# Performance work log

Measured on AMD Instinct MI355X. Metric: run time of the kernel, lower is better.

Reference implementation:

```python
import jax, jax.numpy as jnp
import numpy as np

COMMITMENT_COST = 0.25


def l2norm(x, eps=1e-12):
    # F.normalize along last dim
    n = jnp.linalg.norm(x, axis=-1, keepdims=True)
    return x / jnp.maximum(n, eps)


def vector_quantize(x, codebook, commitment_cost):
    """Euclidean VQ: cdist + argmin, straight-through, VQ loss + perplexity.
    x: (B, N, D), codebook: (K, D)."""
    B, N, D = x.shape
    K = codebook.shape[0]
    flat = x.reshape(-1, D)  # (BN, D)
    # squared euclidean distances via expansion (no (BN,K,D) intermediate)
    d = (jnp.sum(flat * flat, axis=-1, keepdims=True)
         - 2.0 * flat @ codebook.T
         + jnp.sum(codebook * codebook, axis=-1))  # (BN, K)
    idx = jnp.argmin(d, axis=-1)  # (BN,)
    q = codebook[idx]  # (BN, D)
    # VQ losses
    e_latent = jnp.mean((jax.lax.stop_gradient(q) - flat) ** 2)
    q_latent = jnp.mean((q - jax.lax.stop_gradient(flat)) ** 2)
    loss = q_latent + commitment_cost * e_latent
    # perplexity over codebook usage (bincount, not dense one-hot)
    counts = jnp.zeros((K,), flat.dtype).at[idx].add(1.0)
    probs = counts / idx.shape[0]
    perplexity = jnp.exp(-jnp.sum(probs * jnp.log(probs + 1e-10)))
    return idx.reshape(B, N), perplexity, loss


def transform_mfcc(X):
    # wave_embedding.transform_freq: normalize frames, then rfft -> real -> bins 2:40
    Xn = l2norm(X)
    spec = jnp.fft.rfft(Xn, axis=-1).real[..., 2:40]  # (B, N, 38)
    return l2norm(spec)  # mfcc_embedding.norm_fn


def setup_inputs() -> dict:
    key = jax.random.key(0)
    k1, k2, k3 = jax.random.split(key, 3)
    X = jax.random.normal(k1, (16, 4096, 80), dtype=jnp.float32)
    wave_codebook = jax.random.normal(k2, (1024, 80), dtype=jnp.float32)
    mfcc_codebook = jax.random.normal(k3, (256, 38), dtype=jnp.float32)
    return {"X": X, "wave_codebook": wave_codebook, "mfcc_codebook": mfcc_codebook}


def reference(X, wave_codebook, mfcc_codebook):
    K_wave = wave_codebook.shape[0]
    wave_idx, wave_ppl, wave_loss = vector_quantize(X, wave_codebook, COMMITMENT_COST)
    X_mfcc = transform_mfcc(X)
    mfcc_idx, mfcc_ppl, mfcc_loss = vector_quantize(X_mfcc, mfcc_codebook, COMMITMENT_COST)
    mfcc_idx = mfcc_idx + K_wave
    # rearrange stack([wave, mfcc], dim=1): 'b c n -> b (n c)' -> interleave per frame
    B, N = wave_idx.shape
    encodings = jnp.stack([wave_idx, mfcc_idx], axis=-1).reshape(B, 2 * N)
    return encodings, wave_ppl, wave_loss, mfcc_ppl, mfcc_loss
```

## Files before the change

kernel.cpp:

```cpp
#include <hip/hip_runtime.h>
#include <hip/hip_bf16.h>
#include <math.h>


#define NROWS 65536
#define DW    80
#define KW    1024
#define DM    38
#define KM    256

typedef __attribute__((ext_vector_type(8))) short bf16x8;
typedef __attribute__((ext_vector_type(4))) float f32x4;

__device__ __forceinline__ void bf16split(float v, short& h, short& l) {
    __hip_bfloat16 hb = __float2bfloat16(v);
    float hf = __bfloat162float(hb);
    __hip_bfloat16 lb = __float2bfloat16(v - hf);
    h = *(short*)&hb;
    l = *(short*)&lb;
}

__device__ __forceinline__ void bf16split3(float v, short& a, short& b, short& c) {
    __hip_bfloat16 h = __float2bfloat16(v);
    float hf = __bfloat162float(h);
    float r = v - hf;
    __hip_bfloat16 m = __float2bfloat16(r);
    float mf = __bfloat162float(m);
    __hip_bfloat16 lo = __float2bfloat16(r - mf);
    a = *(short*)&h; b = *(short*)&m; c = *(short*)&lo;
}

__device__ __forceinline__ bf16x8 bf8zero() {
    bf16x8 z;
    #pragma unroll
    for (int j = 0; j < 8; ++j) z[j] = 0;
    return z;
}

#define WS_SUMS   0
#define WS_HIST   256
#define WS_CNW    5376
#define WS_CNM    9472
#define WS_CTF    10496
#define WS_CBF    33536
#define WS_CWH    107264
#define WS_CWL    303872

__global__ __launch_bounds__(256) void prep_kernel(
    const float* __restrict__ cbw, const float* __restrict__ cbm,
    float* __restrict__ sums, int* __restrict__ hist,
    float* __restrict__ cn_w, float* __restrict__ cn_m,
    short* __restrict__ ctf, short* __restrict__ cbf,
    short* __restrict__ cwh, short* __restrict__ cwl)
{
    int idx = blockIdx.x * 256 + threadIdx.x;
    if (idx < 12288) {
        const int f = idx;
        const int ct = f / 192, rem = f % 192, s = rem >> 6, l = rem & 63;
        const int code = ct * 16 + (l & 15);
        const int k0 = 32 * s + 8 * (l >> 4);
        bf16x8 h, lo;
        if (k0 < DW) {
            const float4* p = (const float4*)(cbw + (size_t)code * DW + k0);
            float4 u = p[0], v = p[1];
            float fv[8] = {u.x, u.y, u.z, u.w, v.x, v.y, v.z, v.w};
            #pragma unroll
            for (int j = 0; j < 8; ++j) {
                short hh, ll;
                bf16split(fv[j], hh, ll);
                h[j] = hh; lo[j] = ll;
            }
        } else { h = bf8zero(); lo = bf8zero(); }
        *(bf16x8*)&cwh[(size_t)f * 8] = h;
        *(bf16x8*)&cwl[(size_t)f * 8] = lo;
    } else if (idx < 16128) {
        int t = idx - 12288;
        int col, k;
        if (t < 3072) {
            int j = t & 7, l = (t >> 3) & 63, tt = t >> 9;
            col = (tt >> 1) * 16 + (l & 15);
            k = 32 * (tt & 1) + 8 * (l >> 4) + j;
        } else {
            int i2 = t - 3072;
            int j = i2 & 7, l = (i2 >> 3) & 31, ct = i2 >> 8;
            col = ct * 16 + (l & 15);
            k = 64 + 8 * (l >> 4) + j;
        }
        float v = (col < DM)
            ? (float)cos(2.0 * 3.14159265358979323846 * (double)((col + 2) * k) / 80.0)
            : 0.f;
        short a, b, c; bf16split3(v, a, b, c);
        ctf[t] = a; ctf[3840 + t] = b; ctf[7680 + t] = c;
    } else if (idx < 28416) {
        int i3 = idx - 16128;
        int code, k;
        if (i3 < 8192) {
            int j = i3 & 7, l = (i3 >> 3) & 63, ct = i3 >> 9;
            code = ct * 16 + (l & 15);
            k = 8 * (l >> 4) + j;
        } else {
            int i4 = i3 - 8192;
            int j = i4 & 7, l = (i4 >> 3) & 31, ct = i4 >> 8;
            code = ct * 16 + (l & 15);
            k = 32 + 8 * (l >> 4) + j;
        }
        float v = (k < DM) ? cbm[(size_t)code * DM + k] : 0.f;
        short a, b, c; bf16split3(v, a, b, c);
        cbf[i3] = a; cbf[12288 + i3] = b; cbf[24576 + i3] = c;
    } else if (idx < 29440) {
        int i = idx - 28416;
        const float* p = cbw + (size_t)i * DW;
        float s = 0.f;
        for (int k = 0; k < DW; ++k) s = fmaf(p[k], p[k], s);
        cn_w[i] = s;
    } else if (idx < 29696) {
        int i = idx - 29440;
        const float* p = cbm + (size_t)i * DM;
        float s = 0.f;
        for (int j = 0; j < DM; ++j) s = fmaf(p[j], p[j], s);
        cn_m[i] = s;
    } else if (idx < 30976) {
        hist[idx - 29696] = 0;
    } else if (idx == 30976) sums[0] = 0.f;
    else if (idx == 30977)   sums[1] = 0.f;
}

__global__ __launch_bounds__(256, 2) void wave_vq_mfma(
    const float* __restrict__ X, const short* __restrict__ cwh,
    const short* __restrict__ cwl, const float* __restrict__ cn,
    float* __restrict__ out, float* __restrict__ sums)
{
    __shared__ float redw[4];

    const int tid = threadIdx.x;
    const int l   = tid & 63;
    const int qu  = tid >> 6;
    const int c16 = l & 15;
    const int g   = l >> 4;
    const size_t rowbase = (size_t)blockIdx.x * 256 + (size_t)qu * 64;

    bf16x8 Ah[4][3], Al[4][3];
    float xs2[4] = {0.f, 0.f, 0.f, 0.f};
    #pragma unroll
    for (int rt = 0; rt < 4; ++rt) {
        #pragma unroll
        for (int s = 0; s < 3; ++s) {
            const int k0 = 32 * s + 8 * g;
            bf16x8 ah, al;
            if (k0 < DW) {
                const float4* ap =
                    (const float4*)(X + (rowbase + rt * 16 + c16) * DW + k0);
                float4 u = ap[0], w = ap[1];
                float f[8] = {u.x, u.y, u.z, u.w, w.x, w.y, w.z, w.w};
                #pragma unroll
                for (int j = 0; j < 8; ++j) {
                    short hh, ll;
                    bf16split(f[j], hh, ll);
                    ah[j] = hh; al[j] = ll;
                    xs2[rt] = fmaf(f[j], f[j], xs2[rt]);
                }
            } else {
                ah = bf8zero(); al = bf8zero();
            }
            Ah[rt][s] = ah; Al[rt][s] = al;
        }
    }
    #pragma unroll
    for (int rt = 0; rt < 4; ++rt) {
        xs2[rt] += __shfl_xor(xs2[rt], 16, 64);
        xs2[rt] += __shfl_xor(xs2[rt], 32, 64);
    }

    float bd[4][4];
    int   bi[4][4];
    #pragma unroll
    for (int rt = 0; rt < 4; ++rt)
        #pragma unroll
        for (int i = 0; i < 4; ++i) { bd[rt][i] = 3.4e38f; bi[rt][i] = 0; }

    const bf16x8* Hsrc = (const bf16x8*)cwh;
    const bf16x8* Lsrc = (const bf16x8*)cwl;

    bf16x8 pbh[3], pbl[3];
    #pragma unroll
    for (int s = 0; s < 3; ++s) {
        pbh[s] = Hsrc[s * 64 + l];
        pbl[s] = Lsrc[s * 64 + l];
    }
    float pcn = cn[c16];

    #pragma unroll 1
    for (int ct = 0; ct < 64; ++ct) {
        bf16x8 bh[3], bl[3];
        #pragma unroll
        for (int s = 0; s < 3; ++s) { bh[s] = pbh[s]; bl[s] = pbl[s]; }
        const float cnv = pcn;
        if (ct < 63) {
            #pragma unroll
            for (int s = 0; s < 3; ++s) {
                pbh[s] = Hsrc[((ct + 1) * 3 + s) * 64 + l];
                pbl[s] = Lsrc[((ct + 1) * 3 + s) * 64 + l];
            }
            pcn = cn[(ct + 1) * 16 + c16];
        }

        f32x4 acc[4];
        #pragma unroll
        for (int rt = 0; rt < 4; ++rt) acc[rt] = (f32x4){0.f, 0.f, 0.f, 0.f};
        #pragma unroll
        for (int s = 0; s < 3; ++s) {
            #pragma unroll
            for (int rt = 0; rt < 4; ++rt)
                acc[rt] = __builtin_amdgcn_mfma_f32_16x16x32_bf16(Al[rt][s], bl[s], acc[rt], 0, 0, 0);
            #pragma unroll
            for (int rt = 0; rt < 4; ++rt)
                acc[rt] = __builtin_amdgcn_mfma_f32_16x16x32_bf16(Ah[rt][s], bl[s], acc[rt], 0, 0, 0);
            #pragma unroll
            for (int rt = 0; rt < 4; ++rt)
                acc[rt] = __builtin_amdgcn_mfma_f32_16x16x32_bf16(Al[rt][s], bh[s], acc[rt], 0, 0, 0);
            #pragma unroll
            for (int rt = 0; rt < 4; ++rt)
                acc[rt] = __builtin_amdgcn_mfma_f32_16x16x32_bf16(Ah[rt][s], bh[s], acc[rt], 0, 0, 0);
        }
        const int idxbase = ct * 16 + c16;
        #pragma unroll
        for (int rt = 0; rt < 4; ++rt) {
            #pragma unroll
            for (int i = 0; i < 4; ++i) {
                float d = fmaf(-2.f, acc[rt][i], cnv);
                if (d < bd[rt][i]) { bd[rt][i] = d; bi[rt][i] = idxbase; }
            }
        }
    }

    float lw = 0.f;
    #pragma unroll
    for (int rt = 0; rt < 4; ++rt) {
        #pragma unroll
        for (int i = 0; i < 4; ++i) {
            float d = bd[rt][i]; int ix = bi[rt][i];
            #pragma unroll
            for (int m = 1; m < 16; m <<= 1) {
                float d2 = __shfl_xor(d, m, 64);
                int   i2 = __shfl_xor(ix, m, 64);
                if (d2 < d || (d2 == d && i2 < ix)) { d = d2; ix = i2; }
            }
            float xn = __shfl(xs2[rt], (l & 48) + 4 * (l >> 4) + i, 64);
            if (c16 == 0) {
                size_t row = rowbase + rt * 16 + 4 * g + i;
                out[2 * row] = (float)ix;
                lw += d + xn;
            }
        }
    }
    #pragma unroll
    for (int m = 1; m < 64; m <<= 1) lw += __shfl_xor(lw, m, 64);
    if (l == 0) redw[qu] = lw;
    __syncthreads();
    if (tid == 0) atomicAdd(&sums[0], redw[0] + redw[1] + redw[2] + redw[3]);
}

__global__ __launch_bounds__(256, 2) void mfcc_mfma(
    const float* __restrict__ X, const float* __restrict__ cn_m,
    const short* __restrict__ ctf, const short* __restrict__ cbf,
    float* __restrict__ out, float* __restrict__ sums)
{
    __shared__ float XF[4][64 * 49];
    __shared__ float CN[KM];
    __shared__ float red4[4];

    const int tid = threadIdx.x;
    const int l   = tid & 63;
    const int w   = tid >> 6;
    const int c16 = l & 15;
    const int g   = l >> 4;
    const size_t rowbase = (size_t)blockIdx.x * 256 + (size_t)w * 64;

    if (tid < KM) CN[tid] = cn_m[tid];
    __syncthreads();

    float* xfl = &XF[w][0];

    #pragma unroll 1
    for (int rt = 0; rt < 4; ++rt) {
        bf16x8 A0[3], A1[3], A2[3];
        #pragma unroll
        for (int s = 0; s < 3; ++s) {
            const int k0 = 32 * s + 8 * g;
            if (k0 < DW) {
                const float4* ap =
                    (const float4*)(X + (rowbase + rt * 16 + c16) * DW + k0);
                float4 u = ap[0], v = ap[1];
                float f[8] = {u.x, u.y, u.z, u.w, v.x, v.y, v.z, v.w};
                bf16x8 a0, a1, a2;
                #pragma unroll
                for (int j = 0; j < 8; ++j) {
                    short aa, bb, cc;
                    bf16split3(f[j], aa, bb, cc);
                    a0[j] = aa; a1[j] = bb; a2[j] = cc;
                }
                A0[s] = a0; A1[s] = a1; A2[s] = a2;
            } else {
                A0[s] = bf8zero(); A1[s] = bf8zero(); A2[s] = bf8zero();
            }
        }

        f32x4 acc[3];
        #pragma unroll
        for (int ct = 0; ct < 3; ++ct) acc[ct] = (f32x4){0.f, 0.f, 0.f, 0.f};

        #pragma unroll
        for (int s = 0; s < 3; ++s) {
            #pragma unroll
            for (int ct = 0; ct < 3; ++ct) {
                bf16x8 b0, b1, b2;
                if (s < 2) {
                    const int off = ((ct * 2 + s) * 64 + l) * 8;
                    b0 = *(const bf16x8*)&ctf[off];
                    b1 = *(const bf16x8*)&ctf[3840 + off];
                    b2 = *(const bf16x8*)&ctf[7680 + off];
                } else if (l < 32) {
                    const int off = 3072 + (ct * 32 + l) * 8;
                    b0 = *(const bf16x8*)&ctf[off];
                    b1 = *(const bf16x8*)&ctf[3840 + off];
                    b2 = *(const bf16x8*)&ctf[7680 + off];
                } else {
                    b0 = bf8zero(); b1 = bf8zero(); b2 = bf8zero();
                }
                acc[ct] = __builtin_amdgcn_mfma_f32_16x16x32_bf16(A2[s], b0, acc[ct], 0, 0, 0);
                acc[ct] = __builtin_amdgcn_mfma_f32_16x16x32_bf16(A1[s], b1, acc[ct], 0, 0, 0);
                acc[ct] = __builtin_amdgcn_mfma_f32_16x16x32_bf16(A0[s], b2, acc[ct], 0, 0, 0);
                acc[ct] = __builtin_amdgcn_mfma_f32_16x16x32_bf16(A1[s], b0, acc[ct], 0, 0, 0);
                acc[ct] = __builtin_amdgcn_mfma_f32_16x16x32_bf16(A0[s], b1, acc[ct], 0, 0, 0);
                acc[ct] = __builtin_amdgcn_mfma_f32_16x16x32_bf16(A0[s], b0, acc[ct], 0, 0, 0);
            }
        }

        #pragma unroll
        for (int i = 0; i < 4; ++i) {
            float n2 = acc[0][i] * acc[0][i];
            n2 = fmaf(acc[1][i], acc[1][i], n2);
            n2 = fmaf(acc[2][i], acc[2][i], n2);
            #pragma unroll
            for (int m = 1; m < 16; m <<= 1) n2 += __shfl_xor(n2, m, 64);
            float inv = 1.0f / fmaxf(sqrtf(n2), 1e-12f);
            const int row_l = rt * 16 + 4 * g + i;
            #pragma unroll
            for (int ct = 0; ct < 3; ++ct)
                xfl[row_l * 49 + ct * 16 + c16] = acc[ct][i] * inv;
        }
    }
    __syncthreads();

    bf16x8 X0[4][3], X1[4][3];
    #pragma unroll
    for (int rt = 0; rt < 4; ++rt) {
        const int r0 = rt * 16 + c16;
        {
            const float* p = &xfl[r0 * 49 + 8 * g];
            bf16x8 q0, q1, q2;
            #pragma unroll
            for (int j = 0; j < 8; ++j) {
                short aa, bb, cc;
                bf16split3(p[j], aa, bb, cc);
                q0[j] = aa; q1[j] = bb; q2[j] = cc;
            }
            X0[rt][0] = q0; X0[rt][1] = q1; X0[rt][2] = q2;
        }
        if (g < 2) {
            const float* p = &xfl[r0 * 49 + 32 + 8 * g];
            bf16x8 q0, q1, q2;
            #pragma unroll
            for (int j = 0; j < 8; ++j) {
                short aa, bb, cc;
                bf16split3(p[j], aa, bb, cc);
                q0[j] = aa; q1[j] = bb; q2[j] = cc;
            }
            X1[rt][0] = q0; X1[rt][1] = q1; X1[rt][2] = q2;
        } else {
            X1[rt][0] = bf8zero(); X1[rt][1] = bf8zero(); X1[rt][2] = bf8zero();
        }
    }

    float bd[4][4];
    int   bi[4][4];
    #pragma unroll
    for (int rt = 0; rt < 4; ++rt)
        #pragma unroll
        for (int i = 0; i < 4; ++i) { bd[rt][i] = 3.4e38f; bi[rt][i] = 0; }

    #pragma unroll 1
    for (int ct = 0; ct < 16; ++ct) {
        bf16x8 B0[3], B1[3];
        const int off0 = (ct * 64 + l) * 8;
        B0[0] = *(const bf16x8*)&cbf[off0];
        B0[1] = *(const bf16x8*)&cbf[12288 + off0];
        B0[2] = *(const bf16x8*)&cbf[24576 + off0];
        if (l < 32) {
            const int off1 = 8192 + (ct * 32 + l) * 8;
            B1[0] = *(const bf16x8*)&cbf[off1];
            B1[1] = *(const bf16x8*)&cbf[12288 + off1];
            B1[2] = *(const bf16x8*)&cbf[24576 + off1];
        } else {
            B1[0] = bf8zero(); B1[1] = bf8zero(); B1[2] = bf8zero();
        }
        const float cnv = CN[ct * 16 + c16];
        const int idxbase = ct * 16 + c16;
        #pragma unroll
        for (int rt = 0; rt < 4; ++rt) {
            f32x4 a = (f32x4){0.f, 0.f, 0.f, 0.f};
            a = __builtin_amdgcn_mfma_f32_16x16x32_bf16(X0[rt][2], B0[0], a, 0, 0, 0);
            a = __builtin_amdgcn_mfma_f32_16x16x32_bf16(X0[rt][1], B0[1], a, 0, 0, 0);
            a = __builtin_amdgcn_mfma_f32_16x16x32_bf16(X0[rt][0], B0[2], a, 0, 0, 0);
            a = __builtin_amdgcn_mfma_f32_16x16x32_bf16(X1[rt][2], B1[0], a, 0, 0, 0);
            a = __builtin_amdgcn_mfma_f32_16x16x32_bf16(X1[rt][1], B1[1], a, 0, 0, 0);
            a = __builtin_amdgcn_mfma_f32_16x16x32_bf16(X1[rt][0], B1[2], a, 0, 0, 0);
            a = __builtin_amdgcn_mfma_f32_16x16x32_bf16(X0[rt][1], B0[0], a, 0, 0, 0);
            a = __builtin_amdgcn_mfma_f32_16x16x32_bf16(X0[rt][0], B0[1], a, 0, 0, 0);
            a = __builtin_amdgcn_mfma_f32_16x16x32_bf16(X1[rt][1], B1[0], a, 0, 0, 0);
            a = __builtin_amdgcn_mfma_f32_16x16x32_bf16(X1[rt][0], B1[1], a, 0, 0, 0);
            a = __builtin_amdgcn_mfma_f32_16x16x32_bf16(X0[rt][0], B0[0], a, 0, 0, 0);
            a = __builtin_amdgcn_mfma_f32_16x16x32_bf16(X1[rt][0], B1[0], a, 0, 0, 0);
            #pragma unroll
            for (int i = 0; i < 4; ++i) {
                float d = fmaf(-2.f, a[i], cnv);
                if (d < bd[rt][i]) { bd[rt][i] = d; bi[rt][i] = idxbase; }
            }
        }
    }

    float lm = 0.f;
    #pragma unroll
    for (int rt = 0; rt < 4; ++rt) {
        #pragma unroll
        for (int i = 0; i < 4; ++i) {
            float d = bd[rt][i]; int ix = bi[rt][i];
            #pragma unroll
            for (int m = 1; m < 16; m <<= 1) {
                float d2 = __shfl_xor(d, m, 64);
                int   i2 = __shfl_xor(ix, m, 64);
                if (d2 < d || (d2 == d && i2 < ix)) { d = d2; ix = i2; }
            }
            if (c16 == 0) {
                size_t row = rowbase + rt * 16 + 4 * g + i;
                out[2 * row + 1] = (float)(ix + KW);
                lm += d + 1.0f;
            }
        }
    }
    #pragma unroll
    for (int m = 1; m < 64; m <<= 1) lm += __shfl_xor(lm, m, 64);
    if (l == 0) red4[w] = lm;
    __syncthreads();
    if (tid == 0) atomicAdd(&sums[1], red4[0] + red4[1] + red4[2] + red4[3]);
}

__global__ __launch_bounds__(256) void hist_kernel(
    const float* __restrict__ out, int* __restrict__ hist)
{
    __shared__ int h[1280];
    const int tid = threadIdx.x;
    for (int i = tid; i < 1280; i += 256) h[i] = 0;
    __syncthreads();
    const int base = blockIdx.x * 1024;
    for (int rr = tid; rr < 1024; rr += 256) {
        const int r = base + rr;
        atomicAdd(&h[(int)out[2 * r]], 1);
        atomicAdd(&h[1024 + ((int)out[2 * r + 1] - KW)], 1);
    }
    __syncthreads();
    for (int i = tid; i < 1280; i += 256)
        if (h[i]) atomicAdd(&hist[i], h[i]);
}

__global__ __launch_bounds__(256) void finalize_kernel(
    const int* __restrict__ hist, const float* __restrict__ sums,
    float* __restrict__ out)
{
    __shared__ float red[4];
    const int tid = threadIdx.x;
    const bool wv = (blockIdx.x == 0);
    const int K = wv ? KW : KM;
    const int base = wv ? 0 : 1024;
    float s = 0.f;
    for (int i = tid; i < K; i += 256) {
        float p = (float)hist[base + i] * (1.0f / 65536.0f);
        s += p * logf(p + 1e-10f);
    }
    #pragma unroll
    for (int off = 32; off >= 1; off >>= 1) s += __shfl_xor(s, off, 64);
    if ((tid & 63) == 0) red[tid >> 6] = s;
    __syncthreads();
    if (tid == 0) {
        float t = red[0] + red[1] + red[2] + red[3];
        float ppl = expf(-t);
        float denom = wv ? (float)(NROWS * DW) : (float)(NROWS * DM);
        int obase = 2 * NROWS + (wv ? 0 : 2);
        out[obase]     = ppl;
        out[obase + 1] = 1.25f * sums[wv ? 0 : 1] / denom;
    }
}

extern "C" void kernel_launch(void* const* d_in, const int* in_sizes, int n_in,
                              void* d_out, int out_size, void* d_ws, size_t ws_size,
                              hipStream_t stream) {
    const float* X   = (const float*)d_in[0];
    const float* cbw = (const float*)d_in[1];
    const float* cbm = (const float*)d_in[2];
    float* out = (float*)d_out;

    char* ws = (char*)d_ws;
    float* sums = (float*)(ws + WS_SUMS);
    int*   hist = (int*)(ws + WS_HIST);
    float* cn_w = (float*)(ws + WS_CNW);
    float* cn_m = (float*)(ws + WS_CNM);
    short* ctf  = (short*)(ws + WS_CTF);
    short* cbf  = (short*)(ws + WS_CBF);
    short* cwh  = (short*)(ws + WS_CWH);
    short* cwl  = (short*)(ws + WS_CWL);

    prep_kernel<<<122, 256, 0, stream>>>(cbw, cbm, sums, hist, cn_w, cn_m,
                                         ctf, cbf, cwh, cwl);
    wave_vq_mfma<<<NROWS / 256, 256, 0, stream>>>(X, cwh, cwl, cn_w, out, sums);
    mfcc_mfma<<<NROWS / 256, 256, 0, stream>>>(X, cn_m, ctf, cbf, out, sums);
    hist_kernel<<<64, 256, 0, stream>>>(out, hist);
    finalize_kernel<<<2, 256, 0, stream>>>(hist, sums, out);
}
```

Measured before the change: 94.13 us.

## Split codebook search across wave pairs and double the grid size

Both VQ kernels now have two waves share each 64-row group. Each wave scans half of the codebook tiles, and the partial argmins are merged through shared memory before the index write and the loss reduction. Blocks now cover 128 rows instead of 256, so twice as many blocks are launched. The intent is to fill the GPU's compute units with more resident waves. The costs are duplicated X loads and bf16 splitting across the pair, an extra LDS exchange, and a block barrier. In the mfcc kernel the explicit barrier after the CN load was removed, so correctness depends on a later barrier before CN is read.

```diff
diff --git a/kernel.cpp b/kernel.cpp
--- a/kernel.cpp
+++ b/kernel.cpp
@@ -130,14 +130,18 @@
     const short* __restrict__ cwl, const float* __restrict__ cn,
     float* __restrict__ out, float* __restrict__ sums)
 {
-    __shared__ float redw[4];
-
-    const int tid = threadIdx.x;
-    const int l   = tid & 63;
-    const int qu  = tid >> 6;
-    const int c16 = l & 15;
-    const int g   = l >> 4;
-    const size_t rowbase = (size_t)blockIdx.x * 256 + (size_t)qu * 64;
+    __shared__ float sd[2][64][16];
+    __shared__ int   si[2][64][16];
+    __shared__ float redw[2];
+
+    const int tid  = threadIdx.x;
+    const int l    = tid & 63;
+    const int qu   = tid >> 6;
+    const int grp  = qu >> 1;
+    const int half = qu & 1;
+    const int c16  = l & 15;
+    const int g    = l >> 4;
+    const size_t rowbase = (size_t)blockIdx.x * 128 + (size_t)grp * 64;
 
     bf16x8 Ah[4][3], Al[4][3];
     float xs2[4] = {0.f, 0.f, 0.f, 0.f};
@@ -180,22 +184,24 @@
 
     const bf16x8* Hsrc = (const bf16x8*)cwh;
     const bf16x8* Lsrc = (const bf16x8*)cwl;
+    const int ct0 = half * 32;
 
     bf16x8 pbh[3], pbl[3];
     #pragma unroll
     for (int s = 0; s < 3; ++s) {
-        pbh[s] = Hsrc[s * 64 + l];
-        pbl[s] = Lsrc[s * 64 + l];
-    }
-    float pcn = cn[c16];
+        pbh[s] = Hsrc[(ct0 * 3 + s) * 64 + l];
+        pbl[s] = Lsrc[(ct0 * 3 + s) * 64 + l];
+    }
+    float pcn = cn[ct0 * 16 + c16];
 
     #pragma unroll 1
-    for (int ct = 0; ct < 64; ++ct) {
+    for (int ctl = 0; ctl < 32; ++ctl) {
+        const int ct = ct0 + ctl;
         bf16x8 bh[3], bl[3];
         #pragma unroll
         for (int s = 0; s < 3; ++s) { bh[s] = pbh[s]; bl[s] = pbl[s]; }
         const float cnv = pcn;
-        if (ct < 63) {
+        if (ctl < 31) {
             #pragma unroll
             for (int s = 0; s < 3; ++s) {
                 pbh[s] = Hsrc[((ct + 1) * 3 + s) * 64 + l];
@@ -233,31 +239,46 @@
         }
     }
 
-    float lw = 0.f;
-    #pragma unroll
-    for (int rt = 0; rt < 4; ++rt) {
-        #pragma unroll
-        for (int i = 0; i < 4; ++i) {
-            float d = bd[rt][i]; int ix = bi[rt][i];
-            #pragma unroll
-            for (int m = 1; m < 16; m <<= 1) {
-                float d2 = __shfl_xor(d, m, 64);
-                int   i2 = __shfl_xor(ix, m, 64);
-                if (d2 < d || (d2 == d && i2 < ix)) { d = d2; ix = i2; }
-            }
-            float xn = __shfl(xs2[rt], (l & 48) + 4 * (l >> 4) + i, 64);
-            if (c16 == 0) {
-                size_t row = rowbase + rt * 16 + 4 * g + i;
-                out[2 * row] = (float)ix;
-                lw += d + xn;
-            }
-        }
-    }
-    #pragma unroll
-    for (int m = 1; m < 64; m <<= 1) lw += __shfl_xor(lw, m, 64);
-    if (l == 0) redw[qu] = lw;
-    __syncthreads();
-    if (tid == 0) atomicAdd(&sums[0], redw[0] + redw[1] + redw[2] + redw[3]);
+    if (half == 1) {
+        #pragma unroll
+        for (int rt = 0; rt < 4; ++rt)
+            #pragma unroll
+            for (int i = 0; i < 4; ++i) {
+                sd[grp][l][rt * 4 + i] = bd[rt][i];
+                si[grp][l][rt * 4 + i] = bi[rt][i];
+            }
+    }
+    __syncthreads();
+    if (half == 0) {
+        float lw = 0.f;
+        #pragma unroll
+        for (int rt = 0; rt < 4; ++rt) {
+            #pragma unroll
+            for (int i = 0; i < 4; ++i) {
+                float d = bd[rt][i]; int ix = bi[rt][i];
+                float dp = sd[grp][l][rt * 4 + i];
+                int   ip = si[grp][l][rt * 4 + i];
+                if (dp < d || (dp == d && ip < ix)) { d = dp; ix = ip; }
+                #pragma unroll
+                for (int m = 1; m < 16; m <<= 1) {
+                    float d2 = __shfl_xor(d, m, 64);
+                    int   i2 = __shfl_xor(ix, m, 64);
+                    if (d2 < d || (d2 == d && i2 < ix)) { d = d2; ix = i2; }
+                }
+                float xn = __shfl(xs2[rt], (l & 48) + 4 * (l >> 4) + i, 64);
+                if (c16 == 0) {
+                    size_t row = rowbase + rt * 16 + 4 * g + i;
+                    out[2 * row] = (float)ix;
+                    lw += d + xn;
+                }
+            }
+        }
+        #pragma unroll
+        for (int m = 1; m < 64; m <<= 1) lw += __shfl_xor(lw, m, 64);
+        if (l == 0) redw[grp] = lw;
+    }
+    __syncthreads();
+    if (tid == 0) atomicAdd(&sums[0], redw[0] + redw[1]);
 }
 
 __global__ __launch_bounds__(256, 2) void mfcc_mfma(
@@ -265,24 +286,28 @@
     const short* __restrict__ ctf, const short* __restrict__ cbf,
     float* __restrict__ out, float* __restrict__ sums)
 {
-    __shared__ float XF[4][64 * 49];
+    __shared__ float XF[2][64 * 49];
+    __shared__ float sd[2][64][16];
+    __shared__ int   si[2][64][16];
     __shared__ float CN[KM];
-    __shared__ float red4[4];
-
-    const int tid = threadIdx.x;
-    const int l   = tid & 63;
-    const int w   = tid >> 6;
-    const int c16 = l & 15;
-    const int g   = l >> 4;
-    const size_t rowbase = (size_t)blockIdx.x * 256 + (size_t)w * 64;
+    __shared__ float red2[2];
+
+    const int tid  = threadIdx.x;
+    const int l    = tid & 63;
+    const int qu   = tid >> 6;
+    const int grp  = qu >> 1;
+    const int half = qu & 1;
+    const int c16  = l & 15;
+    const int g    = l >> 4;
+    const size_t rowbase = (size_t)blockIdx.x * 128 + (size_t)grp * 64;
 
     if (tid < KM) CN[tid] = cn_m[tid];
-    __syncthreads();
-
-    float* xfl = &XF[w][0];
+
+    float* xfl = &XF[grp][0];
 
     #pragma unroll 1
-    for (int rt = 0; rt < 4; ++rt) {
+    for (int rt2 = 0; rt2 < 2; ++rt2) {
+        const int rt = half * 2 + rt2;
         bf16x8 A0[3], A1[3], A2[3];
         #pragma unroll
         for (int s = 0; s < 3; ++s) {
@@ -390,7 +415,8 @@
         for (int i = 0; i < 4; ++i) { bd[rt][i] = 3.4e38f; bi[rt][i] = 0; }
 
     #pragma unroll 1
-    for (int ct = 0; ct < 16; ++ct) {
+    for (int ctl = 0; ctl < 8; ++ctl) {
+        const int ct = half * 8 + ctl;
         bf16x8 B0[3], B1[3];
         const int off0 = (ct * 64 + l) * 8;
         B0[0] = *(const bf16x8*)&cbf[off0];
@@ -429,30 +455,45 @@
         }
     }
 
-    float lm = 0.f;
-    #pragma unroll
-    for (int rt = 0; rt < 4; ++rt) {
-        #pragma unroll
-        for (int i = 0; i < 4; ++i) {
-            float d = bd[rt][i]; int ix = bi[rt][i];
-            #pragma unroll
-            for (int m = 1; m < 16; m <<= 1) {
-                float d2 = __shfl_xor(d, m, 64);
-                int   i2 = __shfl_xor(ix, m, 64);
-                if (d2 < d || (d2 == d && i2 < ix)) { d = d2; ix = i2; }
-            }
-            if (c16 == 0) {
-                size_t row = rowbase + rt * 16 + 4 * g + i;
-                out[2 * row + 1] = (float)(ix + KW);
-                lm += d + 1.0f;
-            }
-        }
-    }
-    #pragma unroll
-    for (int m = 1; m < 64; m <<= 1) lm += __shfl_xor(lm, m, 64);
-    if (l == 0) red4[w] = lm;
-    __syncthreads();
-    if (tid == 0) atomicAdd(&sums[1], red4[0] + red4[1] + red4[2] + red4[3]);
+    if (half == 1) {
+        #pragma unroll
+        for (int rt = 0; rt < 4; ++rt)
+            #pragma unroll
+            for (int i = 0; i < 4; ++i) {
+                sd[grp][l][rt * 4 + i] = bd[rt][i];
+                si[grp][l][rt * 4 + i] = bi[rt][i];
+            }
+    }
+    __syncthreads();
+    if (half == 0) {
+        float lm = 0.f;
+        #pragma unroll
+        for (int rt = 0; rt < 4; ++rt) {
+            #pragma unroll
+            for (int i = 0; i < 4; ++i) {
+                float d = bd[rt][i]; int ix = bi[rt][i];
+                float dp = sd[grp][l][rt * 4 + i];
+                int   ip = si[grp][l][rt * 4 + i];
+                if (dp < d || (dp == d && ip < ix)) { d = dp; ix = ip; }
+                #pragma unroll
+                for (int m = 1; m < 16; m <<= 1) {
+                    float d2 = __shfl_xor(d, m, 64);
+                    int   i2 = __shfl_xor(ix, m, 64);
+                    if (d2 < d || (d2 == d && i2 < ix)) { d = d2; ix = i2; }
+                }
+                if (c16 == 0) {
+                    size_t row = rowbase + rt * 16 + 4 * g + i;
+                    out[2 * row + 1] = (float)(ix + KW);
+                    lm += d + 1.0f;
+                }
+            }
+        }
+        #pragma unroll
+        for (int m = 1; m < 64; m <<= 1) lm += __shfl_xor(lm, m, 64);
+        if (l == 0) red2[grp] = lm;
+    }
+    __syncthreads();
+    if (tid == 0) atomicAdd(&sums[1], red2[0] + red2[1]);
 }
 
 __global__ __launch_bounds__(256) void hist_kernel(
@@ -521,8 +562,8 @@
 
     prep_kernel<<<122, 256, 0, stream>>>(cbw, cbm, sums, hist, cn_w, cn_m,
                                          ctf, cbf, cwh, cwl);
-    wave_vq_mfma<<<NROWS / 256, 256, 0, stream>>>(X, cwh, cwl, cn_w, out, sums);
-    mfcc_mfma<<<NROWS / 256, 256, 0, stream>>>(X, cn_m, ctf, cbf, out, sums);
+    wave_vq_mfma<<<NROWS / 128, 256, 0, stream>>>(X, cwh, cwl, cn_w, out, sums);
+    mfcc_mfma<<<NROWS / 128, 256, 0, stream>>>(X, cn_m, ctf, cbf, out, sums);
     hist_kernel<<<64, 256, 0, stream>>>(out, hist);
     finalize_kernel<<<2, 256, 0, stream>>>(hist, sums, out);
 }
```

New measurement: 89.73 us. -4.7%, faster.

## Shrink per-wave row tiles to one 16-row tile and raise occupancy

Applied to the files above, without the earlier changes.

Each wave in the wave and mfcc VQ kernels now handles a single 16-row tile instead of four. The grids grow to match (512-thread wave blocks with periodic barriers, smaller mfcc blocks with reduced shared memory), and the histogram kernel gets one row per thread. The aim is to cut register and LDS pressure so more waves fit per CU and more blocks spread across the many CUs. The cost is less reuse of each codebook fragment load across rows, so codebook traffic per row rises about fourfold.

```diff
diff --git a/kernel.cpp b/kernel.cpp
--- a/kernel.cpp
+++ b/kernel.cpp
@@ -35,6 +35,51 @@
     #pragma unroll
     for (int j = 0; j < 8; ++j) z[j] = 0;
     return z;
+}
+
+__device__ __forceinline__ void wvq_tile(
+    const bf16x8 (&Ah)[3], const bf16x8 (&Al)[3],
+    const bf16x8 (&bh)[3], const bf16x8 (&bl)[3],
+    float cnv, int idx0, float (&bd)[4], int (&bi)[4])
+{
+    f32x4 acc = (f32x4){0.f, 0.f, 0.f, 0.f};
+    #pragma unroll
+    for (int s = 0; s < 3; ++s) {
+        acc = __builtin_amdgcn_mfma_f32_16x16x32_bf16(Al[s], bl[s], acc, 0, 0, 0);
+        acc = __builtin_amdgcn_mfma_f32_16x16x32_bf16(Ah[s], bl[s], acc, 0, 0, 0);
+        acc = __builtin_amdgcn_mfma_f32_16x16x32_bf16(Al[s], bh[s], acc, 0, 0, 0);
+        acc = __builtin_amdgcn_mfma_f32_16x16x32_bf16(Ah[s], bh[s], acc, 0, 0, 0);
+    }
+    #pragma unroll
+    for (int i = 0; i < 4; ++i) {
+        float d = fmaf(-2.f, acc[i], cnv);
+        if (d < bd[i]) { bd[i] = d; bi[i] = idx0; }
+    }
+}
+
+__device__ __forceinline__ void mvq_tile(
+    const bf16x8 (&X0)[3], const bf16x8 (&X1)[3],
+    const bf16x8 (&B0)[3], const bf16x8 (&B1)[3],
+    float cnv, int idx0, float (&bd)[4], int (&bi)[4])
+{
+    f32x4 a = (f32x4){0.f, 0.f, 0.f, 0.f};
+    a = __builtin_amdgcn_mfma_f32_16x16x32_bf16(X0[2], B0[0], a, 0, 0, 0);
+    a = __builtin_amdgcn_mfma_f32_16x16x32_bf16(X0[1], B0[1], a, 0, 0, 0);
+    a = __builtin_amdgcn_mfma_f32_16x16x32_bf16(X0[0], B0[2], a, 0, 0, 0);
+    a = __builtin_amdgcn_mfma_f32_16x16x32_bf16(X1[2], B1[0], a, 0, 0, 0);
+    a = __builtin_amdgcn_mfma_f32_16x16x32_bf16(X1[1], B1[1], a, 0, 0, 0);
+    a = __builtin_amdgcn_mfma_f32_16x16x32_bf16(X1[0], B1[2], a, 0, 0, 0);
+    a = __builtin_amdgcn_mfma_f32_16x16x32_bf16(X0[1], B0[0], a, 0, 0, 0);
+    a = __builtin_amdgcn_mfma_f32_16x16x32_bf16(X0[0], B0[1], a, 0, 0, 0);
+    a = __builtin_amdgcn_mfma_f32_16x16x32_bf16(X1[1], B1[0], a, 0, 0, 0);
+    a = __builtin_amdgcn_mfma_f32_16x16x32_bf16(X1[0], B1[1], a, 0, 0, 0);
+    a = __builtin_amdgcn_mfma_f32_16x16x32_bf16(X0[0], B0[0], a, 0, 0, 0);
+    a = __builtin_amdgcn_mfma_f32_16x16x32_bf16(X1[0], B1[0], a, 0, 0, 0);
+    #pragma unroll
+    for (int i = 0; i < 4; ++i) {
+        float d = fmaf(-2.f, a[i], cnv);
+        if (d < bd[i]) { bd[i] = d; bi[i] = idx0; }
+    }
 }
 
 #define WS_SUMS   0
@@ -125,269 +170,217 @@
     else if (idx == 30977)   sums[1] = 0.f;
 }
 
-__global__ __launch_bounds__(256, 2) void wave_vq_mfma(
+__global__ __launch_bounds__(512, 4) void wave_vq_mfma(
     const float* __restrict__ X, const short* __restrict__ cwh,
     const short* __restrict__ cwl, const float* __restrict__ cn,
     float* __restrict__ out, float* __restrict__ sums)
 {
-    __shared__ float redw[4];
+    __shared__ float redw[8];
 
     const int tid = threadIdx.x;
     const int l   = tid & 63;
     const int qu  = tid >> 6;
     const int c16 = l & 15;
     const int g   = l >> 4;
-    const size_t rowbase = (size_t)blockIdx.x * 256 + (size_t)qu * 64;
-
-    bf16x8 Ah[4][3], Al[4][3];
-    float xs2[4] = {0.f, 0.f, 0.f, 0.f};
-    #pragma unroll
-    for (int rt = 0; rt < 4; ++rt) {
+    const size_t rowbase = (size_t)blockIdx.x * 128 + (size_t)qu * 16;
+
+    bf16x8 Ah[3], Al[3];
+    float xs2 = 0.f;
+    #pragma unroll
+    for (int s = 0; s < 3; ++s) {
+        const int k0 = 32 * s + 8 * g;
+        bf16x8 ah, al;
+        if (k0 < DW) {
+            const float4* ap = (const float4*)(X + (rowbase + c16) * DW + k0);
+            float4 u = ap[0], w = ap[1];
+            float f[8] = {u.x, u.y, u.z, u.w, w.x, w.y, w.z, w.w};
+            #pragma unroll
+            for (int j = 0; j < 8; ++j) {
+                short hh, ll;
+                bf16split(f[j], hh, ll);
+                ah[j] = hh; al[j] = ll;
+                xs2 = fmaf(f[j], f[j], xs2);
+            }
+        } else { ah = bf8zero(); al = bf8zero(); }
+        Ah[s] = ah; Al[s] = al;
+    }
+    xs2 += __shfl_xor(xs2, 16, 64);
+    xs2 += __shfl_xor(xs2, 32, 64);
+
+    float bd[4]; int bi[4];
+    #pragma unroll
+    for (int i = 0; i < 4; ++i) { bd[i] = 3.4e38f; bi[i] = 0; }
+
+    const bf16x8* Hp = (const bf16x8*)cwh + l;
+    const bf16x8* Lp = (const bf16x8*)cwl + l;
+
+    bf16x8 b0h[3], b0l[3], b1h[3], b1l[3];
+    float cn0, cn1;
+    #pragma unroll
+    for (int s = 0; s < 3; ++s) { b0h[s] = Hp[s * 64]; b0l[s] = Lp[s * 64]; }
+    cn0 = cn[c16];
+
+    #pragma unroll 1
+    for (int ct = 0; ct < 64; ct += 2) {
+        if ((ct & 15) == 0) __syncthreads();
         #pragma unroll
         for (int s = 0; s < 3; ++s) {
-            const int k0 = 32 * s + 8 * g;
-            bf16x8 ah, al;
-            if (k0 < DW) {
-                const float4* ap =
-                    (const float4*)(X + (rowbase + rt * 16 + c16) * DW + k0);
-                float4 u = ap[0], w = ap[1];
-                float f[8] = {u.x, u.y, u.z, u.w, w.x, w.y, w.z, w.w};
-                #pragma unroll
-                for (int j = 0; j < 8; ++j) {
-                    short hh, ll;
-                    bf16split(f[j], hh, ll);
-                    ah[j] = hh; al[j] = ll;
-                    xs2[rt] = fmaf(f[j], f[j], xs2[rt]);
-                }
-            } else {
-                ah = bf8zero(); al = bf8zero();
-            }
-            Ah[rt][s] = ah; Al[rt][s] = al;
-        }
-    }
-    #pragma unroll
-    for (int rt = 0; rt < 4; ++rt) {
-        xs2[rt] += __shfl_xor(xs2[rt], 16, 64);
-        xs2[rt] += __shfl_xor(xs2[rt], 32, 64);
-    }
-
-    float bd[4][4];
-    int   bi[4][4];
-    #pragma unroll
-    for (int rt = 0; rt < 4; ++rt)
-        #pragma unroll
-        for (int i = 0; i < 4; ++i) { bd[rt][i] = 3.4e38f; bi[rt][i] = 0; }
-
-    const bf16x8* Hsrc = (const bf16x8*)cwh;
-    const bf16x8* Lsrc = (const bf16x8*)cwl;
-
-    bf16x8 pbh[3], pbl[3];
-    #pragma unroll
-    for (int s = 0; s < 3; ++s) {
-        pbh[s] = Hsrc[s * 64 + l];
-        pbl[s] = Lsrc[s * 64 + l];
-    }
-    float pcn = cn[c16];
-
-    #pragma unroll 1
-    for (int ct = 0; ct < 64; ++ct) {
-        bf16x8 bh[3], bl[3];
-        #pragma unroll
-        for (int s = 0; s < 3; ++s) { bh[s] = pbh[s]; bl[s] = pbl[s]; }
-        const float cnv = pcn;
-        if (ct < 63) {
+            b1h[s] = Hp[((ct + 1) * 3 + s) * 64];
+            b1l[s] = Lp[((ct + 1) * 3 + s) * 64];
+        }
+        cn1 = cn[(ct + 1) * 16 + c16];
+        wvq_tile(Ah, Al, b0h, b0l, cn0, ct * 16 + c16, bd, bi);
+        if (ct + 2 < 64) {
             #pragma unroll
             for (int s = 0; s < 3; ++s) {
-                pbh[s] = Hsrc[((ct + 1) * 3 + s) * 64 + l];
-                pbl[s] = Lsrc[((ct + 1) * 3 + s) * 64 + l];
+                b0h[s] = Hp[((ct + 2) * 3 + s) * 64];
+                b0l[s] = Lp[((ct + 2) * 3 + s) * 64];
             }
-            pcn = cn[(ct + 1) * 16 + c16];
-        }
-
-        f32x4 acc[4];
-        #pragma unroll
-        for (int rt = 0; rt < 4; ++rt) acc[rt] = (f32x4){0.f, 0.f, 0.f, 0.f};
-        #pragma unroll
-        for (int s = 0; s < 3; ++s) {
-            #pragma unroll
-            for (int rt = 0; rt < 4; ++rt)
-                acc[rt] = __builtin_amdgcn_mfma_f32_16x16x32_bf16(Al[rt][s], bl[s], acc[rt], 0, 0, 0);
-            #pragma unroll
-            for (int rt = 0; rt < 4; ++rt)
-                acc[rt] = __builtin_amdgcn_mfma_f32_16x16x32_bf16(Ah[rt][s], bl[s], acc[rt], 0, 0, 0);
-            #pragma unroll
-            for (int rt = 0; rt < 4; ++rt)
-                acc[rt] = __builtin_amdgcn_mfma_f32_16x16x32_bf16(Al[rt][s], bh[s], acc[rt], 0, 0, 0);
-            #pragma unroll
-            for (int rt = 0; rt < 4; ++rt)
-                acc[rt] = __builtin_amdgcn_mfma_f32_16x16x32_bf16(Ah[rt][s], bh[s], acc[rt], 0, 0, 0);
-        }
-        const int idxbase = ct * 16 + c16;
-        #pragma unroll
-        for (int rt = 0; rt < 4; ++rt) {
-            #pragma unroll
-            for (int i = 0; i < 4; ++i) {
-                float d = fmaf(-2.f, acc[rt][i], cnv);
-                if (d < bd[rt][i]) { bd[rt][i] = d; bi[rt][i] = idxbase; }
-            }
-        }
+            cn0 = cn[(ct + 2) * 16 + c16];
+        }
+        wvq_tile(Ah, Al, b1h, b1l, cn1, (ct + 1) * 16 + c16, bd, bi);
     }
 
     float lw = 0.f;
     #pragma unroll
-    for (int rt = 0; rt < 4; ++rt) {
-        #pragma unroll
-        for (int i = 0; i < 4; ++i) {
-            float d = bd[rt][i]; int ix = bi[rt][i];
-            #pragma unroll
-            for (int m = 1; m < 16; m <<= 1) {
-                float d2 = __shfl_xor(d, m, 64);
-                int   i2 = __shfl_xor(ix, m, 64);
-                if (d2 < d || (d2 == d && i2 < ix)) { d = d2; ix = i2; }
-            }
-            float xn = __shfl(xs2[rt], (l & 48) + 4 * (l >> 4) + i, 64);
-            if (c16 == 0) {
-                size_t row = rowbase + rt * 16 + 4 * g + i;
-                out[2 * row] = (float)ix;
-                lw += d + xn;
-            }
+    for (int i = 0; i < 4; ++i) {
+        float d = bd[i]; int ix = bi[i];
+        #pragma unroll
+        for (int m = 1; m < 16; m <<= 1) {
+            float d2 = __shfl_xor(d, m, 64);
+            int   i2 = __shfl_xor(ix, m, 64);
+            if (d2 < d || (d2 == d && i2 < ix)) { d = d2; ix = i2; }
+        }
+        float xn = __shfl(xs2, (l & 48) + 4 * g + i, 64);
+        if (c16 == 0) {
+            size_t row = rowbase + 4 * g + i;
+            out[2 * row] = (float)ix;
+            lw += d + xn;
         }
     }
     #pragma unroll
     for (int m = 1; m < 64; m <<= 1) lw += __shfl_xor(lw, m, 64);
     if (l == 0) redw[qu] = lw;
     __syncthreads();
-    if (tid == 0) atomicAdd(&sums[0], redw[0] + redw[1] + redw[2] + redw[3]);
-}
-
-__global__ __launch_bounds__(256, 2) void mfcc_mfma(
+    if (tid == 0) {
+        float t = 0.f;
+        #pragma unroll
+        for (int q = 0; q < 8; ++q) t += redw[q];
+        atomicAdd(&sums[0], t);
+    }
+}
+
+__global__ __launch_bounds__(256, 4) void mfcc_mfma(
     const float* __restrict__ X, const float* __restrict__ cn_m,
     const short* __restrict__ ctf, const short* __restrict__ cbf,
     float* __restrict__ out, float* __restrict__ sums)
 {
-    __shared__ float XF[4][64 * 49];
+    __shared__ float XF[4][16 * 52];
     __shared__ float CN[KM];
     __shared__ float red4[4];
 
     const int tid = threadIdx.x;
     const int l   = tid & 63;
-    const int w   = tid >> 6;
+    const int qu  = tid >> 6;
     const int c16 = l & 15;
     const int g   = l >> 4;
-    const size_t rowbase = (size_t)blockIdx.x * 256 + (size_t)w * 64;
-
-    if (tid < KM) CN[tid] = cn_m[tid];
-    __syncthreads();
-
-    float* xfl = &XF[w][0];
-
-    #pragma unroll 1
-    for (int rt = 0; rt < 4; ++rt) {
-        bf16x8 A0[3], A1[3], A2[3];
-        #pragma unroll
-        for (int s = 0; s < 3; ++s) {
-            const int k0 = 32 * s + 8 * g;
-            if (k0 < DW) {
-                const float4* ap =
-                    (const float4*)(X + (rowbase + rt * 16 + c16) * DW + k0);
-                float4 u = ap[0], v = ap[1];
-                float f[8] = {u.x, u.y, u.z, u.w, v.x, v.y, v.z, v.w};
-                bf16x8 a0, a1, a2;
-                #pragma unroll
-                for (int j = 0; j < 8; ++j) {
-                    short aa, bb, cc;
-                    bf16split3(f[j], aa, bb, cc);
-                    a0[j] = aa; a1[j] = bb; a2[j] = cc;
-                }
-                A0[s] = a0; A1[s] = a1; A2[s] = a2;
-            } else {
-                A0[s] = bf8zero(); A1[s] = bf8zero(); A2[s] = bf8zero();
-            }
-        }
-
-        f32x4 acc[3];
-        #pragma unroll
-        for (int ct = 0; ct < 3; ++ct) acc[ct] = (f32x4){0.f, 0.f, 0.f, 0.f};
-
-        #pragma unroll
-        for (int s = 0; s < 3; ++s) {
-            #pragma unroll
-            for (int ct = 0; ct < 3; ++ct) {
-                bf16x8 b0, b1, b2;
-                if (s < 2) {
-                    const int off = ((ct * 2 + s) * 64 + l) * 8;
-                    b0 = *(const bf16x8*)&ctf[off];
-                    b1 = *(const bf16x8*)&ctf[3840 + off];
-                    b2 = *(const bf16x8*)&ctf[7680 + off];
-                } else if (l < 32) {
-                    const int off = 3072 + (ct * 32 + l) * 8;
-                    b0 = *(const bf16x8*)&ctf[off];
-                    b1 = *(const bf16x8*)&ctf[3840 + off];
-                    b2 = *(const bf16x8*)&ctf[7680 + off];
-                } else {
-                    b0 = bf8zero(); b1 = bf8zero(); b2 = bf8zero();
-                }
-                acc[ct] = __builtin_amdgcn_mfma_f32_16x16x32_bf16(A2[s], b0, acc[ct], 0, 0, 0);
-                acc[ct] = __builtin_amdgcn_mfma_f32_16x16x32_bf16(A1[s], b1, acc[ct], 0, 0, 0);
-                acc[ct] = __builtin_amdgcn_mfma_f32_16x16x32_bf16(A0[s], b2, acc[ct], 0, 0, 0);
-                acc[ct] = __builtin_amdgcn_mfma_f32_16x16x32_bf16(A1[s], b0, acc[ct], 0, 0, 0);
-                acc[ct] = __builtin_amdgcn_mfma_f32_16x16x32_bf16(A0[s], b1, acc[ct], 0, 0, 0);
-                acc[ct] = __builtin_amdgcn_mfma_f32_16x16x32_bf16(A0[s], b0, acc[ct], 0, 0, 0);
-            }
-        }
-
-        #pragma unroll
-        for (int i = 0; i < 4; ++i) {
-            float n2 = acc[0][i] * acc[0][i];
-            n2 = fmaf(acc[1][i], acc[1][i], n2);
-            n2 = fmaf(acc[2][i], acc[2][i], n2);
-            #pragma unroll
-            for (int m = 1; m < 16; m <<= 1) n2 += __shfl_xor(n2, m, 64);
-            float inv = 1.0f / fmaxf(sqrtf(n2), 1e-12f);
-            const int row_l = rt * 16 + 4 * g + i;
-            #pragma unroll
-            for (int ct = 0; ct < 3; ++ct)
-                xfl[row_l * 49 + ct * 16 + c16] = acc[ct][i] * inv;
-        }
-    }
-    __syncthreads();
-
-    bf16x8 X0[4][3], X1[4][3];
-    #pragma unroll
-    for (int rt = 0; rt < 4; ++rt) {
-        const int r0 = rt * 16 + c16;
-        {
-            const float* p = &xfl[r0 * 49 + 8 * g];
-            bf16x8 q0, q1, q2;
+    const size_t rowbase = (size_t)blockIdx.x * 64 + (size_t)qu * 16;
+
+    CN[tid] = cn_m[tid];
+
+    bf16x8 A0[3], A1[3], A2[3];
+    #pragma unroll
+    for (int s = 0; s < 3; ++s) {
+        const int k0 = 32 * s + 8 * g;
+        if (k0 < DW) {
+            const float4* ap = (const float4*)(X + (rowbase + c16) * DW + k0);
+            float4 u = ap[0], v = ap[1];
+            float f[8] = {u.x, u.y, u.z, u.w, v.x, v.y, v.z, v.w};
+            bf16x8 a0, a1, a2;
             #pragma unroll
             for (int j = 0; j < 8; ++j) {
                 short aa, bb, cc;
-                bf16split3(p[j], aa, bb, cc);
-                q0[j] = aa; q1[j] = bb; q2[j] = cc;
+                bf16split3(f[j], aa, bb, cc);
+                a0[j] = aa; a1[j] = bb; a2[j] = cc;
             }
-            X0[rt][0] = q0; X0[rt][1] = q1; X0[rt][2] = q2;
-        }
-        if (g < 2) {
-            const float* p = &xfl[r0 * 49 + 32 + 8 * g];
-            bf16x8 q0, q1, q2;
-            #pragma unroll
-            for (int j = 0; j < 8; ++j) {
-                short aa, bb, cc;
-                bf16split3(p[j], aa, bb, cc);
-                q0[j] = aa; q1[j] = bb; q2[j] = cc;
+            A0[s] = a0; A1[s] = a1; A2[s] = a2;
+        } else { A0[s] = bf8zero(); A1[s] = bf8zero(); A2[s] = bf8zero(); }
+    }
+
+    f32x4 acc[3];
+    #pragma unroll
+    for (int ct = 0; ct < 3; ++ct) acc[ct] = (f32x4){0.f, 0.f, 0.f, 0.f};
+
+    #pragma unroll
+    for (int s = 0; s < 3; ++s) {
+        #pragma unroll
+        for (int ct = 0; ct < 3; ++ct) {
+            bf16x8 b0, b1, b2;
+            if (s < 2) {
+                const int off = ((ct * 2 + s) * 64 + l) * 8;
+                b0 = *(const bf16x8*)&ctf[off];
+                b1 = *(const bf16x8*)&ctf[3840 + off];
+                b2 = *(const bf16x8*)&ctf[7680 + off];
+            } else if (l < 32) {
+                const int off = 3072 + (ct * 32 + l) * 8;
+                b0 = *(const bf16x8*)&ctf[off];
+                b1 = *(const bf16x8*)&ctf[3840 + off];
+                b2 = *(const bf16x8*)&ctf[7680 + off];
+            } else {
+                b0 = bf8zero(); b1 = bf8zero(); b2 = bf8zero();
             }
-            X1[rt][0] = q0; X1[rt][1] = q1; X1[rt][2] = q2;
-        } else {
-            X1[rt][0] = bf8zero(); X1[rt][1] = bf8zero(); X1[rt][2] = bf8zero();
-        }
-    }
-
-    float bd[4][4];
-    int   bi[4][4];
-    #pragma unroll
-    for (int rt = 0; rt < 4; ++rt)
-        #pragma unroll
-        for (int i = 0; i < 4; ++i) { bd[rt][i] = 3.4e38f; bi[rt][i] = 0; }
+            acc[ct] = __builtin_amdgcn_mfma_f32_16x16x32_bf16(A2[s], b0, acc[ct], 0, 0, 0);
+            acc[ct] = __builtin_amdgcn_mfma_f32_16x16x32_bf16(A1[s], b1, acc[ct], 0, 0, 0);
+            acc[ct] = __builtin_amdgcn_mfma_f32_16x16x32_bf16(A0[s], b2, acc[ct], 0, 0, 0);
+            acc[ct] = __builtin_amdgcn_mfma_f32_16x16x32_bf16(A1[s], b0, acc[ct], 0, 0, 0);
+            acc[ct] = __builtin_amdgcn_mfma_f32_16x16x32_bf16(A0[s], b1, acc[ct], 0, 0, 0);
+            acc[ct] = __builtin_amdgcn_mfma_f32_16x16x32_bf16(A0[s], b0, acc[ct], 0, 0, 0);
+        }
+    }
+
+    float* xfl = &XF[qu][0];
+    #pragma unroll
+    for (int i = 0; i < 4; ++i) {
+        float n2 = acc[0][i] * acc[0][i];
+        n2 = fmaf(acc[1][i], acc[1][i], n2);
+        n2 = fmaf(acc[2][i], acc[2][i], n2);
+        #pragma unroll
+        for (int m = 1; m < 16; m <<= 1) n2 += __shfl_xor(n2, m, 64);
+        float inv = 1.0f / fmaxf(sqrtf(n2), 1e-12f);
+        const int row_l = 4 * g + i;
+        #pragma unroll
+        for (int ct = 0; ct < 3; ++ct)
+            xfl[row_l * 52 + ct * 16 + c16] = acc[ct][i] * inv;
+    }
+    __syncthreads();
+
+    bf16x8 X0[3], X1[3];
+    {
+        const float* p = &xfl[c16 * 52 + 8 * g];
+        bf16x8 q0, q1, q2;
+        #pragma unroll
+        for (int j = 0; j < 8; ++j) {
+            short aa, bb, cc;
+            bf16split3(p[j], aa, bb, cc);
+            q0[j] = aa; q1[j] = bb; q2[j] = cc;
+        }
+        X0[0] = q0; X0[1] = q1; X0[2] = q2;
+    }
+    if (g < 2) {
+        const float* p = &xfl[c16 * 52 + 32 + 8 * g];
+        bf16x8 q0, q1, q2;
+        #pragma unroll
+        for (int j = 0; j < 8; ++j) {
+            short aa, bb, cc;
+            bf16split3(p[j], aa, bb, cc);
+            q0[j] = aa; q1[j] = bb; q2[j] = cc;
+        }
+        X1[0] = q0; X1[1] = q1; X1[2] = q2;
+    } else { X1[0] = bf8zero(); X1[1] = bf8zero(); X1[2] = bf8zero(); }
+
+    float bd[4]; int bi[4];
+    #pragma unroll
+    for (int i = 0; i < 4; ++i) { bd[i] = 3.4e38f; bi[i] = 0; }
 
     #pragma unroll 1
     for (int ct = 0; ct < 16; ++ct) {
@@ -401,58 +394,32 @@
             B1[0] = *(const bf16x8*)&cbf[off1];
             B1[1] = *(const bf16x8*)&cbf[12288 + off1];
             B1[2] = *(const bf16x8*)&cbf[24576 + off1];
-        } else {
-            B1[0] = bf8zero(); B1[1] = bf8zero(); B1[2] = bf8zero();
-        }
-        const float cnv = CN[ct * 16 + c16];
-        const int idxbase = ct * 16 + c16;
-        #pragma unroll
-        for (int rt = 0; rt < 4; ++rt) {
-            f32x4 a = (f32x4){0.f, 0.f, 0.f, 0.f};
-            a = __builtin_amdgcn_mfma_f32_16x16x32_bf16(X0[rt][2], B0[0], a, 0, 0, 0);
-            a = __builtin_amdgcn_mfma_f32_16x16x32_bf16(X0[rt][1], B0[1], a, 0, 0, 0);
-            a = __builtin_amdgcn_mfma_f32_16x16x32_bf16(X0[rt][0], B0[2], a, 0, 0, 0);
-            a = __builtin_amdgcn_mfma_f32_16x16x32_bf16(X1[rt][2], B1[0], a, 0, 0, 0);
-            a = __builtin_amdgcn_mfma_f32_16x16x32_bf16(X1[rt][1], B1[1], a, 0, 0, 0);
-            a = __builtin_amdgcn_mfma_f32_16x16x32_bf16(X1[rt][0], B1[2], a, 0, 0, 0);
-            a = __builtin_amdgcn_mfma_f32_16x16x32_bf16(X0[rt][1], B0[0], a, 0, 0, 0);
-            a = __builtin_amdgcn_mfma_f32_16x16x32_bf16(X0[rt][0], B0[1], a, 0, 0, 0);
-            a = __builtin_amdgcn_mfma_f32_16x16x32_bf16(X1[rt][1], B1[0], a, 0, 0, 0);
-            a = __builtin_amdgcn_mfma_f32_16x16x32_bf16(X1[rt][0], B1[1], a, 0, 0, 0);
-            a = __builtin_amdgcn_mfma_f32_16x16x32_bf16(X0[rt][0], B0[0], a, 0, 0, 0);
-            a = __builtin_amdgcn_mfma_f32_16x16x32_bf16(X1[rt][0], B1[0], a, 0, 0, 0);
-            #pragma unroll
-            for (int i = 0; i < 4; ++i) {
-                float d = fmaf(-2.f, a[i], cnv);
-                if (d < bd[rt][i]) { bd[rt][i] = d; bi[rt][i] = idxbase; }
-            }
-        }
+        } else { B1[0] = bf8zero(); B1[1] = bf8zero(); B1[2] = bf8zero(); }
+        mvq_tile(X0, X1, B0, B1, CN[ct * 16 + c16], ct * 16 + c16, bd, bi);
     }
 
     float lm = 0.f;
     #pragma unroll
-    for (int rt = 0; rt < 4; ++rt) {
-        #pragma unroll
-        for (int i = 0; i < 4; ++i) {
-            float d = bd[rt][i]; int ix = bi[rt][i];
-            #pragma unroll
-            for (int m = 1; m < 16; m <<= 1) {
-                float d2 = __shfl_xor(d, m, 64);
-                int   i2 = __shfl_xor(ix, m, 64);
-                if (d2 < d || (d2 == d && i2 < ix)) { d = d2; ix = i2; }
-            }
-            if (c16 == 0) {
-                size_t row = rowbase + rt * 16 + 4 * g + i;
-                out[2 * row + 1] = (float)(ix + KW);
-                lm += d + 1.0f;
-            }
+    for (int i = 0; i < 4; ++i) {
+        float d = bd[i]; int ix = bi[i];
+        #pragma unroll
+        for (int m = 1; m < 16; m <<= 1) {
+            float d2 = __shfl_xor(d, m, 64);
+            int   i2 = __shfl_xor(ix, m, 64);
+            if (d2 < d || (d2 == d && i2 < ix)) { d = d2; ix = i2; }
+        }
+        if (c16 == 0) {
+            size_t row = rowbase + 4 * g + i;
+            out[2 * row + 1] = (float)(ix + KW);
+            lm += d + 1.0f;
         }
     }
     #pragma unroll
     for (int m = 1; m < 64; m <<= 1) lm += __shfl_xor(lm, m, 64);
-    if (l == 0) red4[w] = lm;
-    __syncthreads();
-    if (tid == 0) atomicAdd(&sums[1], red4[0] + red4[1] + red4[2] + red4[3]);
+    if (l == 0) red4[qu] = lm;
+    __syncthreads();
+    if (tid == 0)
+        atomicAdd(&sums[1], red4[0] + red4[1] + red4[2] + red4[3]);
 }
 
 __global__ __launch_bounds__(256) void hist_kernel(
@@ -462,12 +429,10 @@
     const int tid = threadIdx.x;
     for (int i = tid; i < 1280; i += 256) h[i] = 0;
     __syncthreads();
-    const int base = blockIdx.x * 1024;
-    for (int rr = tid; rr < 1024; rr += 256) {
-        const int r = base + rr;
-        atomicAdd(&h[(int)out[2 * r]], 1);
-        atomicAdd(&h[1024 + ((int)out[2 * r + 1] - KW)], 1);
-    }
+    const int r = blockIdx.x * 256 + tid;
+    float2 e = *(const float2*)&out[2 * r];
+    atomicAdd(&h[(int)e.x], 1);
+    atomicAdd(&h[1024 + ((int)e.y - KW)], 1);
     __syncthreads();
     for (int i = tid; i < 1280; i += 256)
         if (h[i]) atomicAdd(&hist[i], h[i]);
@@ -521,8 +486,8 @@
 
     prep_kernel<<<122, 256, 0, stream>>>(cbw, cbm, sums, hist, cn_w, cn_m,
                                          ctf, cbf, cwh, cwl);
-    wave_vq_mfma<<<NROWS / 256, 256, 0, stream>>>(X, cwh, cwl, cn_w, out, sums);
-    mfcc_mfma<<<NROWS / 256, 256, 0, stream>>>(X, cn_m, ctf, cbf, out, sums);
-    hist_kernel<<<64, 256, 0, stream>>>(out, hist);
+    wave_vq_mfma<<<NROWS / 128, 512, 0, stream>>>(X, cwh, cwl, cn_w, out, sums);
+    mfcc_mfma<<<NROWS / 64, 256, 0, stream>>>(X, cn_m, ctf, cbf, out, sums);
+    hist_kernel<<<NROWS / 256, 256, 0, stream>>>(out, hist);
     finalize_kernel<<<2, 256, 0, stream>>>(hist, sums, out);
 }
```

New measurement: 106.5 us. 1.13x slower.
